# Kernel tuning notes

Measured on AMD Instinct MI355X. Metric: run time of the kernel, lower is better.

## Reference

```python
import jax, jax.numpy as jnp
import numpy as np

L_MAX = 3          # max output angular momentum (L_max in the module)
N_L_IN = 4         # input l = 0..3, all with sigma = +1
Q = 16             # q_max per input block
N_SAMPLES = 4000   # number of atomic environments (samples)


def _combos():
    # Mirrors CGIteration.initialize: for each (l1,s1=1) x (l2,s2=1) pair,
    # emit L in |l1-l2|..min(l1+l2, L_max), S = (-1)^(l1+l2+L).
    out = []
    for l1 in range(N_L_IN):
        for l2 in range(N_L_IN):
            for L in range(abs(l1 - l2), min(l1 + l2, L_MAX) + 1):
                out.append((l1, l2, L, (-1) ** (l1 + l2 + L)))
    return out


def setup_inputs() -> dict:
    key = jax.random.key(0)
    ks = jax.random.split(key, 9)
    inp = {}
    for l in range(N_L_IN):
        inp[f"x1_l{l}"] = jax.random.normal(ks[l], (N_SAMPLES, 2 * l + 1, Q), dtype=jnp.float32)
        inp[f"x2_l{l}"] = jax.random.normal(ks[4 + l], (N_SAMPLES, 2 * l + 1, Q), dtype=jnp.float32)
    # Padded Clebsch-Gordan coefficient table: cg_coeffs[l1, l2, L, m1, m2, M]
    # (slices [:2l1+1, :2l2+1, :2L+1] are used; padding is ignored).
    inp["cg_coeffs"] = jax.random.normal(
        ks[8], (N_L_IN, N_L_IN, L_MAX + 1, 2 * N_L_IN - 1, 2 * N_L_IN - 1, 2 * L_MAX + 1),
        dtype=jnp.float32)
    return inp


def _forward(x1, x2, cg_coeffs):
    # One species; per-(L,S) output block lists, then concat along properties.
    blocks = {}
    for l1, l2, L, S in _combos():
        C = cg_coeffs[l1, l2, L, :2 * l1 + 1, :2 * l2 + 1, :2 * L + 1]  # [m1, m2, M]
        # cg.combine with 'full' selected_features == full cartesian (q1, q2)
        # outer product: out[n, M, q1, q2] = sum_{m1,m2} C[m1,m2,M] x1[n,m1,q1] x2[n,m2,q2]
        b = jnp.einsum('nip,njq,ijM->nMpq', x1[l1], x2[l2], C)
        b = b.reshape(b.shape[0], 2 * L + 1, -1)  # [n, 2L+1, q1*q2]
        blocks.setdefault((L, S), []).append(b)
    outs = []
    for key in sorted(blocks.keys()):
        v = jnp.concatenate(blocks[key], axis=-1)      # cat along 'mixed' properties
        outs.append(v.reshape(v.shape[0], -1))         # flatten (m, properties)
    return jnp.concatenate(outs, axis=-1)              # [n, 39936]


def reference(x1_l0, x1_l1, x1_l2, x1_l3, x2_l0, x2_l1, x2_l2, x2_l3, cg_coeffs):
    x1 = [x1_l0, x1_l1, x1_l2, x1_l3]
    x2 = [x2_l0, x2_l1, x2_l2, x2_l3]
    return _forward(x1, x2, cg_coeffs)
```

## Files before the change

### kernel.cpp

```cpp
#include <hip/hip_runtime.h>


namespace {

constexpr int NC = 34;

struct CInfo { int l1, l2, L, pbase, outbase, mstride; };
struct CTable { CInfo c[NC]; int packed_total; int outsize; };

constexpr CTable build_table() {
  CTable t{};
  int nb[4][2] = {};
  for (int l1 = 0; l1 < 4; ++l1)
    for (int l2 = 0; l2 < 4; ++l2) {
      int lo = l1 > l2 ? l1 - l2 : l2 - l1;
      int hi = (l1 + l2 < 3) ? l1 + l2 : 3;
      for (int L = lo; L <= hi; ++L)
        nb[L][((l1 + l2 + L) & 1) ? 0 : 1]++;
    }
  int keyoff[4][2] = {};
  int off = 0;
  for (int L = 0; L < 4; ++L)
    for (int s = 0; s < 2; ++s) {
      keyoff[L][s] = off;
      off += (2 * L + 1) * 256 * nb[L][s];
    }
  t.outsize = off;
  int blk[4][2] = {};
  int idx = 0, pb = 0;
  for (int l1 = 0; l1 < 4; ++l1)
    for (int l2 = 0; l2 < 4; ++l2) {
      int lo = l1 > l2 ? l1 - l2 : l2 - l1;
      int hi = (l1 + l2 < 3) ? l1 + l2 : 3;
      for (int L = lo; L <= hi; ++L) {
        int s = ((l1 + l2 + L) & 1) ? 0 : 1;
        pb = (pb + 15) & ~15;
        t.c[idx].l1 = l1; t.c[idx].l2 = l2; t.c[idx].L = L;
        t.c[idx].pbase = pb;
        t.c[idx].outbase = keyoff[L][s] + blk[L][s] * 256;
        t.c[idx].mstride = 256 * nb[L][s];
        blk[L][s]++;
        pb += (2 * l1 + 1) * (2 * l2 + 1) * (2 * L + 1);
        ++idx;
      }
    }
  t.packed_total = pb;
  return t;
}

constexpr CTable CTAB = build_table();
static_assert(CTAB.outsize == 39936, "output layout mismatch");
static_assert(CTAB.packed_total <= 4096, "packed cg exceeds 16KB");

template <int CI>
__device__ __forceinline__ void pack_combo(const float* __restrict__ cg,
                                           float* __restrict__ cgp, int tid) {
  if constexpr (CI < NC) {
    constexpr CInfo c = CTAB.c[CI];
    constexpr int D2 = 2 * c.l2 + 1, DL = 2 * c.L + 1;
    constexpr int SZ = (2 * c.l1 + 1) * D2 * DL;
    for (int tt = tid; tt < SZ; tt += 256) {
      int M = tt % DL, ij = tt / DL;
      int j = ij % D2, i = ij / D2;
      cgp[c.pbase + tt] =
          cg[((((c.l1 * 4 + c.l2) * 4 + c.L) * 7 + i) * 7 + j) * 7 + M];
    }
    pack_combo<CI + 1>(cg, cgp, tid);
  }
}

__global__ void pack_cg_kernel(const float* __restrict__ cg,
                               float* __restrict__ cgp) {
  pack_combo<0>(cg, cgp, (int)threadIdx.x);
}

template <int CI>
__device__ __forceinline__ void run_combos(const float* __restrict__ cgp,
                                           const float (&x1r)[16],
                                           const float (&x2r)[16],
                                           float* __restrict__ outn) {
  if constexpr (CI < NC) {
    constexpr CInfo c = CTAB.c[CI];
    constexpr int D1 = 2 * c.l1 + 1, D2 = 2 * c.l2 + 1, DL = 2 * c.L + 1;
    constexpr int R1 = c.l1 * c.l1, R2 = c.l2 * c.l2;
    float acc[DL];
#pragma unroll
    for (int M = 0; M < DL; ++M) acc[M] = 0.f;
#pragma unroll
    for (int i = 0; i < D1; ++i) {
#pragma unroll
      for (int j = 0; j < D2; ++j) {
        const float ab = x1r[R1 + i] * x2r[R2 + j];
#pragma unroll
        for (int M = 0; M < DL; ++M)
          acc[M] = fmaf(cgp[c.pbase + (i * D2 + j) * DL + M], ab, acc[M]);
      }
    }
#pragma unroll
    for (int M = 0; M < DL; ++M)
      outn[c.outbase + M * c.mstride] = acc[M];
    run_combos<CI + 1>(cgp, x1r, x2r, outn);
  }
}

__global__ __launch_bounds__(256) void cg_main(
    const float* __restrict__ x1_0, const float* __restrict__ x2_0,
    const float* __restrict__ x1_1, const float* __restrict__ x2_1,
    const float* __restrict__ x1_2, const float* __restrict__ x2_2,
    const float* __restrict__ x1_3, const float* __restrict__ x2_3,
    const float* __restrict__ cgp_, float* __restrict__ out) {
  const float* cgp = (const float*)__builtin_assume_aligned(cgp_, 256);
  __shared__ float x1s[16][16];
  __shared__ float x2s[16][16];
  const int tid = (int)threadIdx.x;
  const int n = (int)blockIdx.x;
  const int r = tid >> 4, col = tid & 15;
  const float* s1; const float* s2; int ri;
  if (r < 1)      { s1 = x1_0 + n * 16;  s2 = x2_0 + n * 16;  ri = r; }
  else if (r < 4) { s1 = x1_1 + n * 48;  s2 = x2_1 + n * 48;  ri = r - 1; }
  else if (r < 9) { s1 = x1_2 + n * 80;  s2 = x2_2 + n * 80;  ri = r - 4; }
  else            { s1 = x1_3 + n * 112; s2 = x2_3 + n * 112; ri = r - 9; }
  x1s[r][col] = s1[ri * 16 + col];
  x2s[r][col] = s2[ri * 16 + col];
  __syncthreads();
  float x1r[16], x2r[16];
#pragma unroll
  for (int k = 0; k < 16; ++k) {
    x1r[k] = x1s[k][r];
    x2r[k] = x2s[k][col];
  }
  float* outn = out + (size_t)n * (size_t)CTAB.outsize + tid;
  run_combos<0>(cgp, x1r, x2r, outn);
}

}

extern "C" void kernel_launch(void* const* d_in, const int* in_sizes, int n_in,
                              void* d_out, int out_size, void* d_ws,
                              size_t ws_size, hipStream_t stream) {
  const float* x1[4];
  const float* x2[4];
  if (in_sizes[1] == in_sizes[0]) {
    for (int l = 0; l < 4; ++l) {
      x1[l] = (const float*)d_in[2 * l];
      x2[l] = (const float*)d_in[2 * l + 1];
    }
  } else {
    for (int l = 0; l < 4; ++l) {
      x1[l] = (const float*)d_in[l];
      x2[l] = (const float*)d_in[4 + l];
    }
  }
  const float* cg = (const float*)d_in[8];
  float* out = (float*)d_out;
  float* cgp = (float*)d_ws;

  const int n = in_sizes[0] / 16;

  pack_cg_kernel<<<1, 256, 0, stream>>>(cg, cgp);
  cg_main<<<n, 256, 0, stream>>>(x1[0], x2[0], x1[1], x2[1], x1[2], x2[2],
                                 x1[3], x2[3], cgp, out);
}
```

Baseline: 168.8 us.

## Split each sample across four single-wave blocks and stagger combo order

Each sample is now handled by four 64-thread blocks, one wavefront each, instead of one 256-thread block. Each lane loads its x1/x2 values straight from global memory, so the shared-memory staging and the __syncthreads barrier are gone. Odd blocks walk the 34 combos in a rotated order, which spreads write traffic across different output regions at the same moment. The cost is four times as many blocks, the code path is instantiated twice (larger code size), and the global loads are less coalesced.

```diff
diff --git a/kernel.cpp b/kernel.cpp
--- a/kernel.cpp
+++ b/kernel.cpp
@@ -74,13 +74,13 @@
   pack_combo<0>(cg, cgp, (int)threadIdx.x);
 }
 
-template <int CI>
+template <int ROT, int K>
 __device__ __forceinline__ void run_combos(const float* __restrict__ cgp,
                                            const float (&x1r)[16],
                                            const float (&x2r)[16],
                                            float* __restrict__ outn) {
-  if constexpr (CI < NC) {
-    constexpr CInfo c = CTAB.c[CI];
+  if constexpr (K < NC) {
+    constexpr CInfo c = CTAB.c[(K + ROT) % NC];
     constexpr int D1 = 2 * c.l1 + 1, D2 = 2 * c.l2 + 1, DL = 2 * c.L + 1;
     constexpr int R1 = c.l1 * c.l1, R2 = c.l2 * c.l2;
     float acc[DL];
@@ -99,38 +99,41 @@
 #pragma unroll
     for (int M = 0; M < DL; ++M)
       outn[c.outbase + M * c.mstride] = acc[M];
-    run_combos<CI + 1>(cgp, x1r, x2r, outn);
+    run_combos<ROT, K + 1>(cgp, x1r, x2r, outn);
   }
 }
 
-__global__ __launch_bounds__(256) void cg_main(
+__global__ __launch_bounds__(64) void cg_main(
     const float* __restrict__ x1_0, const float* __restrict__ x2_0,
     const float* __restrict__ x1_1, const float* __restrict__ x2_1,
     const float* __restrict__ x1_2, const float* __restrict__ x2_2,
     const float* __restrict__ x1_3, const float* __restrict__ x2_3,
     const float* __restrict__ cgp_, float* __restrict__ out) {
   const float* cgp = (const float*)__builtin_assume_aligned(cgp_, 256);
-  __shared__ float x1s[16][16];
-  __shared__ float x2s[16][16];
-  const int tid = (int)threadIdx.x;
-  const int n = (int)blockIdx.x;
-  const int r = tid >> 4, col = tid & 15;
-  const float* s1; const float* s2; int ri;
-  if (r < 1)      { s1 = x1_0 + n * 16;  s2 = x2_0 + n * 16;  ri = r; }
-  else if (r < 4) { s1 = x1_1 + n * 48;  s2 = x2_1 + n * 48;  ri = r - 1; }
-  else if (r < 9) { s1 = x1_2 + n * 80;  s2 = x2_2 + n * 80;  ri = r - 4; }
-  else            { s1 = x1_3 + n * 112; s2 = x2_3 + n * 112; ri = r - 9; }
-  x1s[r][col] = s1[ri * 16 + col];
-  x2s[r][col] = s2[ri * 16 + col];
-  __syncthreads();
+  const int lane = (int)threadIdx.x;
+  const int id = (int)blockIdx.x;
+  const int n = id >> 2, a = id & 3;
+  const int p = a * 4 + (lane >> 4), q = lane & 15;
   float x1r[16], x2r[16];
+  {
+    const float* b1[4] = {x1_0 + n * 16, x1_1 + n * 48, x1_2 + n * 80,
+                          x1_3 + n * 112};
+    const float* b2[4] = {x2_0 + n * 16, x2_1 + n * 48, x2_2 + n * 80,
+                          x2_3 + n * 112};
 #pragma unroll
-  for (int k = 0; k < 16; ++k) {
-    x1r[k] = x1s[k][r];
-    x2r[k] = x2s[k][col];
+    for (int l = 0; l < 4; ++l) {
+#pragma unroll
+      for (int i = 0; i < 2 * l + 1; ++i) {
+        x1r[l * l + i] = b1[l][i * 16 + p];
+        x2r[l * l + i] = b2[l][i * 16 + q];
+      }
+    }
   }
-  float* outn = out + (size_t)n * (size_t)CTAB.outsize + tid;
-  run_combos<0>(cgp, x1r, x2r, outn);
+  float* outn = out + (size_t)n * (size_t)CTAB.outsize + a * 64 + lane;
+  if (id & 1)
+    run_combos<17, 0>(cgp, x1r, x2r, outn);
+  else
+    run_combos<0, 0>(cgp, x1r, x2r, outn);
 }
 
 }
@@ -158,6 +161,6 @@
   const int n = in_sizes[0] / 16;
 
   pack_cg_kernel<<<1, 256, 0, stream>>>(cg, cgp);
-  cg_main<<<n, 256, 0, stream>>>(x1[0], x2[0], x1[1], x2[1], x1[2], x2[2],
-                                 x1[3], x2[3], cgp, out);
+  cg_main<<<4 * n, 64, 0, stream>>>(x1[0], x2[0], x1[1], x2[1], x1[2],
+                                    x2[2], x1[3], x2[3], cgp, out);
 }
```

After: 276.0 us. +63.5%, slower.
